# Kernel optimization log

Hardware: AMD Instinct MI355X
Metric: run time of the kernel (lower is better)

## Reference

```python
import jax, jax.numpy as jnp
import numpy as np

N, C, SI, VI, H, R = 10000, 2, 128, 16, 4, 32
SH, VH = SI // H, VI // H  # 32, 4
EPS = 1e-8

def _vnorm(x, axis):
    # clamped L2 norm, matches _norm_no_nan
    return jnp.sqrt(jnp.clip(jnp.sum(x * x, axis=axis), EPS, None))

def _gvp_full(s, v, wh, ws_w, ws_b, wv, wsv_w, wsv_b):
    # GVP with activations=(silu, sigmoid), vector_gate=True, vi=vo
    vh = jnp.swapaxes(v, -1, -2) @ wh            # [..., 3, h]
    vn = _vnorm(vh, -2)                          # [..., h]
    so = jnp.concatenate([s, vn], -1) @ ws_w + ws_b
    vo = jnp.swapaxes(vh @ wv, -1, -2)           # [..., vo, 3]
    gate = jax.nn.sigmoid(jax.nn.sigmoid(so) @ wsv_w + wsv_b)
    return jax.nn.silu(so), vo * gate[..., None]

def setup_inputs():
    key = jax.random.key(0)
    ks = iter(jax.random.split(key, 40))
    def lin(i, o):
        return jax.random.normal(next(ks), (i, o), jnp.float32) / np.sqrt(i)
    def bias(o):
        return 0.02 * jax.random.normal(next(ks), (o,), jnp.float32)
    inp = {}
    inp['s'] = jax.random.normal(next(ks), (N, C, SI), jnp.float32)
    inp['v'] = jax.random.normal(next(ks), (N, C, VI, 3), jnp.float32)
    # weight_proj: GVP((SI,VI)->(R,0)), no activations; h_dim = max(VI,0) = VI
    inp['wp_wh'] = lin(VI, VI); inp['wp_ws_w'] = lin(VI + SI, R); inp['wp_ws_b'] = bias(R)
    # to_q/k/v: GVP((SI,VI)->(SI,VI)), silu/sigmoid, vector_gate; h_dim = VI
    for p in ('q', 'k', 'vv'):
        inp[p + '_wh'] = lin(VI, VI)
        inp[p + '_ws_w'] = lin(VI + SI, SI); inp[p + '_ws_b'] = bias(SI)
        inp[p + '_wv'] = lin(VI, VI)
        inp[p + '_wsv_w'] = lin(SI, VI); inp[p + '_wsv_b'] = bias(VI)
    # attn_gvp_long: GVP((2*SH, 2*VH) -> (1,0)), no activations; h_dim = 2*VH
    inp['attn_wh'] = lin(2 * VH, 2 * VH)
    inp['attn_ws_w'] = lin(2 * VH + 2 * SH, 1); inp['attn_ws_b'] = bias(1)
    return inp

def reference(s, v, wp_wh, wp_ws_w, wp_ws_b,
              q_wh, q_ws_w, q_ws_b, q_wv, q_wsv_w, q_wsv_b,
              k_wh, k_ws_w, k_ws_b, k_wv, k_wsv_w, k_wsv_b,
              vv_wh, vv_ws_w, vv_ws_b, vv_wv, vv_wsv_w, vv_wsv_b,
              attn_wh, attn_ws_w, attn_ws_b):
    n, c = s.shape[:2]
    # ---- Compress: softmax-pool N -> R anchors ----
    vh = jnp.swapaxes(v, -1, -2) @ wp_wh          # [N,C,3,VI]
    vn = _vnorm(vh, -2)                            # [N,C,VI]
    pw = jnp.concatenate([s, vn], -1) @ wp_ws_w + wp_ws_b  # [N,C,R]
    pw = jax.nn.softmax(pw, axis=0)                # softmax over nodes
    s_g = jnp.einsum('nca,ncs->acs', pw, s)        # [R,C,SI] (includes transpose(0,1))
    v_g = jnp.einsum('nca,ncvd->acvd', pw, v)      # [R,C,VI,3]
    # ---- q from nodes, k/v from anchors ----
    qs, qv = _gvp_full(s, v, q_wh, q_ws_w, q_ws_b, q_wv, q_wsv_w, q_wsv_b)
    ks, kv = _gvp_full(s_g, v_g, k_wh, k_ws_w, k_ws_b, k_wv, k_wsv_w, k_wsv_b)
    vs, vv_ = _gvp_full(s_g, v_g, vv_wh, vv_ws_w, vv_ws_b, vv_wv, vv_wsv_w, vv_wsv_b)
    qs = qs.reshape(n, c, H, SH); qv = qv.reshape(n, c, H, VH, 3)
    ks = ks.reshape(R, c, H, SH); kv = kv.reshape(R, c, H, VH, 3)
    vs = vs.reshape(R, c, H, SH); vv_ = vv_.reshape(R, c, H, VH, 3)
    # ---- attention GVP on cat(q, k): split weights instead of materializing concat ----
    wh_q, wh_k = attn_wh[:VH], attn_wh[VH:]        # wh @ cat(qv,kv) = qv@wh_q + kv@wh_k
    qh = jnp.swapaxes(qv, -1, -2) @ wh_q           # [N,C,H,3,2VH]
    kh = jnp.swapaxes(kv, -1, -2) @ wh_k           # [R,C,H,3,2VH]
    vn2 = _vnorm(qh[:, None] + kh[None], -2)       # [N,R,C,H,2VH]
    ws_q = attn_ws_w[:SH]; ws_k = attn_ws_w[SH:2 * SH]; ws_n = attn_ws_w[2 * SH:]
    e = (qs @ ws_q)[:, None] + (ks @ ws_k)[None] + vn2 @ ws_n + attn_ws_b  # [N,R,C,H,1]
    e = e[..., 0] / np.sqrt(SH)
    alpha = jax.nn.softmax(e, axis=1)              # softmax over anchors (dim=1)
    # ---- Broadcast: weighted sum of anchor values ----
    out_s = jnp.einsum('nrch,rchd->nchd', alpha, vs).reshape(n, c, SI)
    out_v = jnp.einsum('nrch,rchde->nchde', alpha, vv_).reshape(n, c, VI, 3)
    return out_s, out_v
```

## Files before the change

### kernel.cpp

```cpp
#include <hip/hip_runtime.h>
#include <hip/hip_bf16.h>


#define N_  10000
#define C_  2
#define SI_ 128
#define VI_ 16
#define H_  4
#define R_  32
#define SH_ 32
#define VH_ 4
#define NC_ (N_*C_)

typedef const float* __restrict__ fptr;

__device__ __forceinline__ float sigm(float x){ return 1.f/(1.f+__expf(-x)); }

#define OFF_LG   0
#define OFF_EQH  640000
#define OFF_SG   2640000
#define OFF_TKH  2651520
#define OFF_TEK  2657664
#define OFF_TVS  2657920
#define OFF_TVV  2666112

#define SGSTRIDE_ 180

__global__ __launch_bounds__(256) void kA(
    fptr s, fptr v,
    fptr wp_wh, fptr wp_ws_w, fptr wp_ws_b,
    fptr q_wh, fptr q_ws_w, fptr q_ws_b, fptr q_wv, fptr q_wsv_w, fptr q_wsv_b,
    fptr attn_wh, fptr attn_ws_w,
    float* __restrict__ pexp, float* __restrict__ eqh,
    float* __restrict__ sgz)
{
  __shared__ __align__(16) float ARENA[160*12];
  __shared__ __align__(16) float VVs[8*48];
  __shared__ __align__(16) float VHQ[8*48];
  __shared__ __align__(16) float SO[8*128];
  __shared__ __align__(16) float GATE[8*16];
  __shared__ __align__(16) float QV[8*48];
  float* const XT  = ARENA;
  float* const SIG = ARENA;

  const int tid  = threadIdx.x;
  const int row0 = blockIdx.x * 8;

  if (blockIdx.x == 0){
    for (int i = tid; i < 64*SGSTRIDE_; i += 256) sgz[i] = 0.f;
  }

  for (int idx = tid; idx < 8*128; idx += 256){
    int r = idx >> 7, j = idx & 127;
    XT[j*12 + r] = s[(row0+r)*128 + j];
  }
  for (int idx = tid; idx < 8*48; idx += 256){
    int r = idx / 48, k = idx - r*48;
    VVs[r*48 + k] = v[(row0+r)*48 + k];
  }
  __syncthreads();

  {
    int r = tid >> 5, ii = tid & 31, path = ii >> 4, i = ii & 15;
    fptr wh = path ? wp_wh : q_wh;
    float h0=0.f, h1=0.f, h2=0.f;
    #pragma unroll
    for (int j = 0; j < 16; j++){
      float w = wh[j*16 + i];
      h0 = fmaf(VVs[r*48 + j*3 + 0], w, h0);
      h1 = fmaf(VVs[r*48 + j*3 + 1], w, h1);
      h2 = fmaf(VVs[r*48 + j*3 + 2], w, h2);
    }
    float vn = sqrtf(fmaxf(h0*h0 + h1*h1 + h2*h2, 1e-8f));
    if (!path){
      VHQ[r*48 +  0 + i] = h0;
      VHQ[r*48 + 16 + i] = h1;
      VHQ[r*48 + 32 + i] = h2;
      XT[(128+i)*12 + r] = vn;
    } else {
      XT[(144+i)*12 + r] = vn;
    }
  }
  __syncthreads();

  const int colA = tid & 127, rgA = tid >> 7;
  float acc[4];
  {
    float bqs = q_ws_b[colA];
    #pragma unroll
    for (int k = 0; k < 4; k++) acc[k] = bqs;
    #pragma unroll 8
    for (int j = 0; j < 144; j++){
      float w = q_ws_w[j*128 + colA];
      float4 x0 = *(const float4*)&XT[j*12 + rgA*4];
      acc[0] = fmaf(x0.x, w, acc[0]); acc[1] = fmaf(x0.y, w, acc[1]);
      acc[2] = fmaf(x0.z, w, acc[2]); acc[3] = fmaf(x0.w, w, acc[3]);
    }
  }
  {
    const int col = tid & 31, rg = tid >> 5;
    float a0 = wp_ws_b[col];
    #pragma unroll 8
    for (int j = 0; j < 144; j++){
      int jj = (j < 128) ? j : (j + 16);
      a0 = fmaf(XT[jj*12 + rg], wp_ws_w[j*32 + col], a0);
    }
    const int c = rg & 1, n = (row0 + rg) >> 1;
    pexp[(c*32 + col)*N_ + n] = __expf(a0);
  }
  __syncthreads();

  #pragma unroll
  for (int k = 0; k < 4; k++){
    float so = acc[k];
    float sg_ = sigm(so);
    SIG[(rgA*4 + k)*128 + colA] = sg_;
    SO [(rgA*4 + k)*128 + colA] = so * sg_;
  }
  __syncthreads();

  if (tid < 128){
    const int r = tid >> 4, g = tid & 15;
    float ga = q_wsv_b[g];
    #pragma unroll 8
    for (int o = 0; o < 128; o += 4){
      float4 s4 = *(const float4*)&SIG[r*128 + o];
      ga = fmaf(s4.x, q_wsv_w[(o+0)*16 + g], ga);
      ga = fmaf(s4.y, q_wsv_w[(o+1)*16 + g], ga);
      ga = fmaf(s4.z, q_wsv_w[(o+2)*16 + g], ga);
      ga = fmaf(s4.w, q_wsv_w[(o+3)*16 + g], ga);
    }
    GATE[r*16 + g] = sigm(ga);
  } else if (tid < 160){
    const int t2 = tid - 128, r = t2 >> 2, h = t2 & 3;
    float e = 0.f;
    #pragma unroll
    for (int t = 0; t < 32; t++)
      e = fmaf(SO[r*128 + h*32 + t], attn_ws_w[t], e);
    eqh[(row0 + r)*100 + h] = e;
  }
  __syncthreads();

  for (int t = tid; t < 8*48; t += 256){
    int r = t / 48, k = t - r*48, i = k / 3, d = k - i*3;
    float a = 0.f;
    #pragma unroll
    for (int j = 0; j < 16; j++)
      a = fmaf(VHQ[r*48 + d*16 + j], q_wv[j*16 + i], a);
    QV[r*48 + k] = a * GATE[r*16 + i];
  }
  __syncthreads();

  for (int t = tid; t < 8*96; t += 256){
    int r = t / 96, k = t - r*96;
    int h = k / 24, rem = k - h*24, d = rem >> 3, ee = rem & 7;
    float a = 0.f;
    #pragma unroll
    for (int i = 0; i < 4; i++)
      a = fmaf(QV[r*48 + (h*4 + i)*3 + d], attn_wh[i*8 + ee], a);
    eqh[(row0 + r)*100 + 8 + k] = a;
  }
}

__global__ __launch_bounds__(256) void kAccum(const float* __restrict__ pexp,
                                              fptr s, fptr v,
                                              float* __restrict__ sg)
{
  const int b = blockIdx.x;
  const int c = b & 1, ah = (b >> 1) & 1, chunk = b >> 2;
  const int n0 = chunk * 50;
  const int tid = threadIdx.x;
  const int ag = tid >> 6, dl = tid & 63;
  const int abase = ah*16 + ag*4;

  const float* pb = pexp + (c*32 + abase)*N_;
  float acc[4][3] = {};
  float dn[4] = {};

  #pragma unroll 2
  for (int n = n0; n < n0 + 50; n++){
    const int rc = n*2 + c;
    float pw[4];
    #pragma unroll
    for (int aa = 0; aa < 4; aa++){
      pw[aa] = pb[aa*N_ + n];
      dn[aa] += pw[aa];
    }
    #pragma unroll
    for (int dd = 0; dd < 3; dd++){
      int d = dl + 64*dd;
      if (d < 176){
        float xv = (d < 128) ? s[rc*128 + d] : v[rc*48 + d - 128];
        #pragma unroll
        for (int aa = 0; aa < 4; aa++)
          acc[aa][dd] = fmaf(pw[aa], xv, acc[aa][dd]);
      }
    }
  }
  #pragma unroll
  for (int aa = 0; aa < 4; aa++){
    const int base = (c*32 + abase + aa)*SGSTRIDE_;
    #pragma unroll
    for (int dd = 0; dd < 3; dd++){
      int d = dl + 64*dd;
      if (d < 176) atomicAdd(&sg[base + d], acc[aa][dd]);
    }
    if (dl == 0) atomicAdd(&sg[base + 176], dn[aa]);
  }
}

__global__ __launch_bounds__(256) void kSmall(
    const float* __restrict__ sg,
    fptr k_wh, fptr k_ws_w, fptr k_ws_b, fptr k_wv, fptr k_wsv_w, fptr k_wsv_b,
    fptr vv_wh, fptr vv_ws_w, fptr vv_ws_b, fptr vv_wv, fptr vv_wsv_w, fptr vv_wsv_b,
    fptr attn_wh, fptr attn_ws_w,
    float* __restrict__ tkh, float* __restrict__ tek,
    float* __restrict__ tvs, float* __restrict__ tvv)
{
  const int b = blockIdx.x, r = b >> 1, c = b & 1;
  const int tid = threadIdx.x;
  __shared__ float X[176];
  __shared__ float VN[2][16];
  __shared__ float VH[2][48];
  __shared__ float SOk[128], SOv[128];
  __shared__ float G[2][16];
  __shared__ float KV[48];

  if (tid < 176){
    const float* p = sg + (c*32 + r)*SGSTRIDE_;
    X[tid] = p[tid] / p[176];
  }
  __syncthreads();

  if (tid < 32){
    int path = tid >> 4, i = tid & 15;
    fptr wh = path ? vv_wh : k_wh;
    float h0=0.f, h1=0.f, h2=0.f;
    #pragma unroll
    for (int j = 0; j < 16; j++){
      float w = wh[j*16 + i];
      h0 = fmaf(X[128 + j*3 + 0], w, h0);
      h1 = fmaf(X[128 + j*3 + 1], w, h1);
      h2 = fmaf(X[128 + j*3 + 2], w, h2);
    }
    VH[path][ 0 + i] = h0; VH[path][16 + i] = h1; VH[path][32 + i] = h2;
    VN[path][i] = sqrtf(fmaxf(h0*h0 + h1*h1 + h2*h2, 1e-8f));
  }
  __syncthreads();

  {
    int path = tid >> 7, col = tid & 127;
    fptr W  = path ? vv_ws_w : k_ws_w;
    fptr Bb = path ? vv_ws_b : k_ws_b;
    float so = Bb[col];
    for (int j = 0; j < 128; j++) so = fmaf(X[j], W[j*128 + col], so);
    #pragma unroll
    for (int i = 0; i < 16; i++)  so = fmaf(VN[path][i], W[(128+i)*128 + col], so);
    (path ? SOv : SOk)[col] = so;
  }
  __syncthreads();

  if (tid < 32){
    int path = tid >> 4, g = tid & 15;
    fptr Wsv = path ? vv_wsv_w : k_wsv_w;
    fptr Bsv = path ? vv_wsv_b : k_wsv_b;
    const float* SOp = path ? SOv : SOk;
    float ga = Bsv[g];
    for (int o = 0; o < 128; o++)
      ga = fmaf(sigm(SOp[o]), Wsv[o*16 + g], ga);
    G[path][g] = sigm(ga);
  } else if (tid < 36){
    int h = tid - 32;
    float e = 0.f;
    #pragma unroll
    for (int t = 0; t < 32; t++){
      float so = SOk[h*32 + t];
      e = fmaf(so * sigm(so), attn_ws_w[32 + t], e);
    }
    tek[(r*2 + c)*4 + h] = e;
  } else if (tid >= 64 && tid < 192){
    int o = tid - 64;
    float so = SOv[o];
    tvs[(r*2 + c)*128 + o] = so * sigm(so);
  }
  __syncthreads();

  if (tid < 96){
    int path = tid / 48, k = tid % 48, i = k / 3, d = k - i*3;
    fptr Wv = path ? vv_wv : k_wv;
    float vo = 0.f;
    #pragma unroll
    for (int j = 0; j < 16; j++)
      vo = fmaf(VH[path][d*16 + j], Wv[j*16 + i], vo);
    float gv = vo * G[path][i];
    if (path == 0) KV[k] = gv;
    else {
      int h = i >> 2, ii = i & 3;
      tvv[(((r*2 + c)*4 + h)*4 + ii)*3 + d] = gv;
    }
  }
  __syncthreads();

  if (tid < 96){
    int h = tid / 24, rem = tid % 24, d = rem >> 3, ee = rem & 7;
    float a = 0.f;
    #pragma unroll
    for (int i = 0; i < 4; i++)
      a = fmaf(KV[(h*4 + i)*3 + d], attn_wh[(4 + i)*8 + ee], a);
    tkh[((r*2 + c)*4 + h)*24 + d*8 + ee] = a;
  }
}

__global__ __launch_bounds__(512, 1) void kAttn(
    const float* __restrict__ eqh,
    const float* __restrict__ tkh, const float* __restrict__ tek,
    const float* __restrict__ tvs, const float* __restrict__ tvv,
    fptr attn_ws_w, fptr attn_ws_b,
    float* __restrict__ out)
{
  __shared__ __align__(16) float KH[6144];
  __shared__ __align__(16) float EK[256];
  __shared__ __align__(16) float VS[256*36];
  __shared__ __align__(16) float VVt[3072];
  const int tid = threadIdx.x;

  for (int i = tid; i < 6144; i += 512) KH[i] = tkh[i];
  if (tid < 256) EK[tid] = tek[tid];
  for (int i = tid; i < 8192; i += 512){ int base = i >> 5, t = i & 31; VS[base*36 + t] = tvs[i]; }
  for (int i = tid; i < 3072; i += 512) VVt[i] = tvv[i];

  float wsn[8];
  #pragma unroll
  for (int ee = 0; ee < 8; ee++) wsn[ee] = attn_ws_w[64 + ee];
  const float wb = attn_ws_b[0];
  __syncthreads();

  const int row = blockIdx.x*128 + (tid >> 2);
  const int h = tid & 3;
  if (row < NC_){
    const int c = row & 1;
    const float eq = eqh[row*100 + h];
    float qh[24];
    {
      const float4* qp = (const float4*)&eqh[row*100 + 8 + h*24];
      #pragma unroll
      for (int k = 0; k < 6; k++){
        float4 t4 = qp[k];
        qh[k*4+0] = t4.x; qh[k*4+1] = t4.y; qh[k*4+2] = t4.z; qh[k*4+3] = t4.w;
      }
    }
    float4 accs4[8];
    float4 accv4[3];
    #pragma unroll
    for (int q = 0; q < 8; q++) accs4[q] = make_float4(0.f,0.f,0.f,0.f);
    #pragma unroll
    for (int q = 0; q < 3; q++) accv4[q] = make_float4(0.f,0.f,0.f,0.f);
    float den = 0.f;

    #pragma unroll
    for (int r = 0; r < 32; r++){
      const int base = (r*2 + c)*4 + h;
      const float* khp = &KH[base*24];
      float en = 0.f;
      #pragma unroll
      for (int ee = 0; ee < 8; ee++){
        float a0 = qh[ee]      + khp[ee];
        float a1 = qh[8 + ee]  + khp[8 + ee];
        float a2 = qh[16 + ee] + khp[16 + ee];
        en = fmaf(sqrtf(fmaxf(a0*a0 + a1*a1 + a2*a2, 1e-8f)), wsn[ee], en);
      }
      const float w = __expf((eq + EK[base] + en + wb) * 0.17677669529663687f);
      den += w;
      const float4* vp4 = (const float4*)&VS[base*36];
      #pragma unroll
      for (int q = 0; q < 8; q++){
        float4 t4 = vp4[q];
        accs4[q].x = fmaf(w, t4.x, accs4[q].x);
        accs4[q].y = fmaf(w, t4.y, accs4[q].y);
        accs4[q].z = fmaf(w, t4.z, accs4[q].z);
        accs4[q].w = fmaf(w, t4.w, accs4[q].w);
      }
      const float4* vv4 = (const float4*)&VVt[base*12];
      #pragma unroll
      for (int q = 0; q < 3; q++){
        float4 t4 = vv4[q];
        accv4[q].x = fmaf(w, t4.x, accv4[q].x);
        accv4[q].y = fmaf(w, t4.y, accv4[q].y);
        accv4[q].z = fmaf(w, t4.z, accv4[q].z);
        accv4[q].w = fmaf(w, t4.w, accv4[q].w);
      }
    }
    const float inv = 1.f / den;
    float4* po = (float4*)&out[row*128 + h*32];
    #pragma unroll
    for (int q = 0; q < 8; q++){
      float4 t4 = accs4[q];
      t4.x *= inv; t4.y *= inv; t4.z *= inv; t4.w *= inv;
      po[q] = t4;
    }
    float4* pv = (float4*)&out[NC_*128 + row*48 + h*12];
    #pragma unroll
    for (int q = 0; q < 3; q++){
      float4 t4 = accv4[q];
      t4.x *= inv; t4.y *= inv; t4.z *= inv; t4.w *= inv;
      pv[q] = t4;
    }
  }
}

extern "C" void kernel_launch(void* const* d_in, const int* in_sizes, int n_in,
                              void* d_out, int out_size, void* d_ws, size_t ws_size,
                              hipStream_t stream)
{
  fptr s        = (fptr)d_in[0];
  fptr v        = (fptr)d_in[1];
  fptr wp_wh    = (fptr)d_in[2];
  fptr wp_ws_w  = (fptr)d_in[3];
  fptr wp_ws_b  = (fptr)d_in[4];
  fptr q_wh     = (fptr)d_in[5];
  fptr q_ws_w   = (fptr)d_in[6];
  fptr q_ws_b   = (fptr)d_in[7];
  fptr q_wv     = (fptr)d_in[8];
  fptr q_wsv_w  = (fptr)d_in[9];
  fptr q_wsv_b  = (fptr)d_in[10];
  fptr k_wh     = (fptr)d_in[11];
  fptr k_ws_w   = (fptr)d_in[12];
  fptr k_ws_b   = (fptr)d_in[13];
  fptr k_wv     = (fptr)d_in[14];
  fptr k_wsv_w  = (fptr)d_in[15];
  fptr k_wsv_b  = (fptr)d_in[16];
  fptr vv_wh    = (fptr)d_in[17];
  fptr vv_ws_w  = (fptr)d_in[18];
  fptr vv_ws_b  = (fptr)d_in[19];
  fptr vv_wv    = (fptr)d_in[20];
  fptr vv_wsv_w = (fptr)d_in[21];
  fptr vv_wsv_b = (fptr)d_in[22];
  fptr attn_wh  = (fptr)d_in[23];
  fptr attn_ws_w= (fptr)d_in[24];
  fptr attn_ws_b= (fptr)d_in[25];

  float* ws   = (float*)d_ws;
  float* pexp = ws + OFF_LG;
  float* eqh  = ws + OFF_EQH;
  float* sg   = ws + OFF_SG;
  float* tkh  = ws + OFF_TKH;
  float* tek  = ws + OFF_TEK;
  float* tvs  = ws + OFF_TVS;
  float* tvv  = ws + OFF_TVV;

  kA<<<NC_/8, 256, 0, stream>>>(s, v, wp_wh, wp_ws_w, wp_ws_b,
                                q_wh, q_ws_w, q_ws_b, q_wv, q_wsv_w, q_wsv_b,
                                attn_wh, attn_ws_w, pexp, eqh, sg);
  kAccum<<<800, 256, 0, stream>>>(pexp, s, v, sg);
  kSmall<<<64, 256, 0, stream>>>(sg,
                                 k_wh, k_ws_w, k_ws_b, k_wv, k_wsv_w, k_wsv_b,
                                 vv_wh, vv_ws_w, vv_ws_b, vv_wv, vv_wsv_w, vv_wsv_b,
                                 attn_wh, attn_ws_w, tkh, tek, tvs, tvv);
  kAttn<<<(NC_ + 127)/128, 512, 0, stream>>>(eqh, tkh, tek, tvs, tvv,
                                             attn_ws_w, attn_ws_b, (float*)d_out);
}
```

Before: 241.6 us.

## Double-buffer projection weight tiles through shared memory with register prefetch

Measured after the change: 757.4 us. 3.14x slower.

```diff
diff --git a/kernel.cpp b/kernel.cpp
--- a/kernel.cpp
+++ b/kernel.cpp
@@ -40,11 +40,21 @@
   __shared__ __align__(16) float SO[8*128];
   __shared__ __align__(16) float GATE[8*16];
   __shared__ __align__(16) float QV[8*48];
+  __shared__ __align__(16) float WQ[2][16*128];
+  __shared__ __align__(16) float WP[2][16*32];
   float* const XT  = ARENA;
   float* const SIG = ARENA;
 
   const int tid  = threadIdx.x;
   const int row0 = blockIdx.x * 8;
+
+  float4 wq0a, wq0b, wp0;
+  {
+    const float4* qsrc = (const float4*)q_ws_w;
+    wq0a = qsrc[tid];
+    wq0b = qsrc[tid + 256];
+    if (tid < 128) wp0 = ((const float4*)wp_ws_w)[tid];
+  }
 
   if (blockIdx.x == 0){
     for (int i = tid; i < 64*SGSTRIDE_; i += 256) sgz[i] = 0.f;
@@ -57,6 +67,11 @@
   for (int idx = tid; idx < 8*48; idx += 256){
     int r = idx / 48, k = idx - r*48;
     VVs[r*48 + k] = v[(row0+r)*48 + k];
+  }
+  {
+    float4* dq = (float4*)WQ[0];
+    dq[tid] = wq0a; dq[tid + 256] = wq0b;
+    if (tid < 128) ((float4*)WP[0])[tid] = wp0;
   }
   __syncthreads();
 
@@ -84,31 +99,54 @@
   __syncthreads();
 
   const int colA = tid & 127, rgA = tid >> 7;
+  const int colB = tid & 31,  rgB = tid >> 5;
   float acc[4];
   {
     float bqs = q_ws_b[colA];
     #pragma unroll
     for (int k = 0; k < 4; k++) acc[k] = bqs;
-    #pragma unroll 8
-    for (int j = 0; j < 144; j++){
-      float w = q_ws_w[j*128 + colA];
-      float4 x0 = *(const float4*)&XT[j*12 + rgA*4];
-      acc[0] = fmaf(x0.x, w, acc[0]); acc[1] = fmaf(x0.y, w, acc[1]);
-      acc[2] = fmaf(x0.z, w, acc[2]); acc[3] = fmaf(x0.w, w, acc[3]);
-    }
-  }
-  {
-    const int col = tid & 31, rg = tid >> 5;
-    float a0 = wp_ws_b[col];
-    #pragma unroll 8
-    for (int j = 0; j < 144; j++){
-      int jj = (j < 128) ? j : (j + 16);
-      a0 = fmaf(XT[jj*12 + rg], wp_ws_w[j*32 + col], a0);
-    }
-    const int c = rg & 1, n = (row0 + rg) >> 1;
-    pexp[(c*32 + col)*N_ + n] = __expf(a0);
-  }
-  __syncthreads();
+  }
+  float a0 = wp_ws_b[colB];
+  int cur = 0;
+  const float* xbA = &XT[rgA*4];
+
+  for (int t = 0; t < 9; t++){
+    float4 nqa, nqb, npa;
+    if (t < 8){
+      const float4* qsrc = (const float4*)(q_ws_w + (t+1)*16*128);
+      nqa = qsrc[tid];
+      nqb = qsrc[tid + 256];
+      if (tid < 128) npa = ((const float4*)(wp_ws_w + (t+1)*16*32))[tid];
+    }
+    {
+      const float* wq = WQ[cur];
+      const int j0 = t*16;
+      #pragma unroll
+      for (int jl = 0; jl < 16; jl++){
+        float w = wq[jl*128 + colA];
+        float4 x = *(const float4*)(xbA + (j0+jl)*12);
+        acc[0] = fmaf(x.x, w, acc[0]); acc[1] = fmaf(x.y, w, acc[1]);
+        acc[2] = fmaf(x.z, w, acc[2]); acc[3] = fmaf(x.w, w, acc[3]);
+      }
+      const float* wp = WP[cur];
+      const int xrow0 = (t == 8) ? (j0 + 16) : j0;
+      #pragma unroll
+      for (int jl = 0; jl < 16; jl++)
+        a0 = fmaf(XT[(xrow0 + jl)*12 + rgB], wp[jl*32 + colB], a0);
+    }
+    if (t < 8){
+      float4* dq = (float4*)WQ[cur ^ 1];
+      dq[tid] = nqa; dq[tid + 256] = nqb;
+      if (tid < 128) ((float4*)WP[cur ^ 1])[tid] = npa;
+    }
+    __syncthreads();
+    cur ^= 1;
+  }
+
+  {
+    const int c = rgB & 1, n = (row0 + rgB) >> 1;
+    pexp[(c*32 + colB)*N_ + n] = __expf(a0);
+  }
 
   #pragma unroll
   for (int k = 0; k < 4; k++){
```
